# Kernel tuning notes

Measured on AMD Instinct MI355X. Metric: run time of the kernel, lower is better.

Reference implementation:

```python
import jax, jax.numpy as jnp
import numpy as np

D = 256        # d_model
NH = 8         # nhead
L = 2          # num_layers
FF = 1024      # dim_feedforward
HD = D // NH   # head dim
LN_EPS = 1e-5
M_EPS = 1e-9


def setup_inputs() -> dict:
    key = jax.random.key(0)
    ks = jax.random.split(key, 8)
    B, N, E = 8, 1024, 16384
    s = 0.02
    inp = {
        "H": jax.random.normal(ks[0], (B, N, D), jnp.float32),
        "edge_index": jax.random.randint(ks[1], (B, 2, E), 0, N),
        "m": jax.random.uniform(ks[2], (B, E), jnp.float32),
        # transformer encoder params, stacked over layers
        "Wqkv": jax.random.normal(ks[3], (L, 3 * D, D), jnp.float32) * s,
        "bqkv": jnp.zeros((L, 3 * D), jnp.float32),
        "Wo": jax.random.normal(ks[4], (L, D, D), jnp.float32) * s,
        "bo": jnp.zeros((L, D), jnp.float32),
        "ln1_w": jnp.ones((L, D), jnp.float32),
        "ln1_b": jnp.zeros((L, D), jnp.float32),
        "W1": jax.random.normal(ks[5], (L, FF, D), jnp.float32) * s,
        "b1": jnp.zeros((L, FF), jnp.float32),
        "W2": jax.random.normal(ks[6], (L, D, FF), jnp.float32) * s,
        "b2": jnp.zeros((L, D), jnp.float32),
        "ln2_w": jnp.ones((L, D), jnp.float32),
        "ln2_b": jnp.zeros((L, D), jnp.float32),
        "lnf_w": jnp.ones((D,), jnp.float32),
        "lnf_b": jnp.zeros((D,), jnp.float32),
    }
    return inp


def layer_norm(x, w, b):
    mu = jnp.mean(x, axis=-1, keepdims=True)
    var = jnp.mean(jnp.square(x - mu), axis=-1, keepdims=True)
    return (x - mu) * jax.lax.rsqrt(var + LN_EPS) * w + b


def build_bias(edge_index, m, N):
    # per-graph: -inf everywhere, 0 on diag, log(m+eps) symmetrically on edges
    bias = jnp.full((N, N), -jnp.inf, jnp.float32)
    d = jnp.arange(N)
    bias = bias.at[d, d].set(0.0)
    bv = jnp.log(m + M_EPS)
    row, col = edge_index[0], edge_index[1]
    bias = bias.at[row, col].set(bv)
    bias = bias.at[col, row].set(bv)
    return bias


def mha(x, bias, Wqkv, bqkv, Wo, bo):
    B, N, d = x.shape
    qkv = x @ Wqkv.T + bqkv                          # [B,N,3D]
    q, k, v = jnp.split(qkv, 3, axis=-1)
    def heads(t):
        return t.reshape(B, N, NH, HD).transpose(0, 2, 1, 3)  # [B,NH,N,HD]
    q, k, v = heads(q), heads(k), heads(v)
    scores = jnp.einsum("bhnd,bhmd->bhnm", q, k) / np.sqrt(HD)
    scores = scores + bias[:, None]                  # same bias for all heads
    attn = jax.nn.softmax(scores, axis=-1)
    out = jnp.einsum("bhnm,bhmd->bhnd", attn, v)
    out = out.transpose(0, 2, 1, 3).reshape(B, N, d)
    return out @ Wo.T + bo


def reference(H, edge_index, m, Wqkv, bqkv, Wo, bo, ln1_w, ln1_b, W1, b1,
              W2, b2, ln2_w, ln2_b, lnf_w, lnf_b):
    B, N, _ = H.shape
    bias = jax.vmap(lambda ei, mm: build_bias(ei, mm, N))(edge_index, m)  # [B,N,N]
    x = H
    for l in range(L):  # small fixed layer count
        a = mha(x, bias, Wqkv[l], bqkv[l], Wo[l], bo[l])
        x = layer_norm(x + a, ln1_w[l], ln1_b[l])
        f = jax.nn.gelu(x @ W1[l].T + b1[l], approximate=False) @ W2[l].T + b2[l]
        x = layer_norm(x + f, ln2_w[l], ln2_b[l])
    return layer_norm(x, lnf_w, lnf_b)
```

## Files before the change

kernel.cpp:

```cpp
#include <hip/hip_runtime.h>
#include <hip/hip_bf16.h>
#include <math.h>

typedef __bf16 bf16_t;
typedef __attribute__((ext_vector_type(8))) __bf16 bf16x8;
typedef __attribute__((ext_vector_type(4))) __bf16 bf16x4;
typedef __attribute__((ext_vector_type(4))) float f32x4;

#define BATCH 8
#define NTOK 1024
#define NEDGE 16384
#define CAP 96

__device__ __forceinline__ void gload_lds16(const void* g, void* l) {
  __builtin_amdgcn_global_load_lds(
      (const __attribute__((address_space(1))) unsigned int*)(uintptr_t)g,
      (__attribute__((address_space(3))) unsigned int*)(unsigned int)(uintptr_t)l,
      16, 0, 0);
}

__global__ void k_pre(int4* __restrict__ cnt,
                      const float* __restrict__ H, const float* __restrict__ Wqkv,
                      const float* __restrict__ Wo, const float* __restrict__ W1,
                      const float* __restrict__ W2, bf16_t* __restrict__ xb,
                      bf16_t* __restrict__ wqkvb, bf16_t* __restrict__ wob,
                      bf16_t* __restrict__ w1b, bf16_t* __restrict__ w2b) {
  int i = blockIdx.x * 256 + threadIdx.x;
  if (blockIdx.x < 8) {
    int4 z = {0, 0, 0, 0};
    cnt[i] = z;
  }
  const float* s; bf16_t* d; int off;
  if (i < 524288)      { s = H;    d = xb;    off = i; }
  else if (i < 622592) { s = Wqkv; d = wqkvb; off = i - 524288; }
  else if (i < 655360) { s = Wo;   d = wob;   off = i - 622592; }
  else if (i < 786432) { s = W1;   d = w1b;   off = i - 655360; }
  else if (i < 917504) { s = W2;   d = w2b;   off = i - 786432; }
  else return;
  float4 v = ((const float4*)s)[off];
  bf16x4 o;
  o[0] = (bf16_t)v.x; o[1] = (bf16_t)v.y; o[2] = (bf16_t)v.z; o[3] = (bf16_t)v.w;
  ((bf16x4*)d)[off] = o;
}

__global__ void k_scatter2(const int* __restrict__ ei, int* __restrict__ cnt,
                           int* __restrict__ ent) {
  int idx = blockIdx.x * 256 + threadIdx.x;
  if (idx >= BATCH * NEDGE) return;
  int b = idx >> 14;
  int e = idx & (NEDGE - 1);
  const int* eb = ei + (size_t)b * 2 * NEDGE;
  int r = eb[e], c = eb[NEDGE + e];
  int rowr = (b << 10) + r, rowc = (b << 10) + c;
  int q = atomicAdd(cnt + rowr, 1);
  if (q < CAP) ent[rowr * CAP + q] = ((e + 1) << 10) | c;
  q = atomicAdd(cnt + rowc, 1);
  if (q < CAP) ent[rowc * CAP + q] = ((NEDGE + e + 1) << 10) | r;
}

__global__ __launch_bounds__(256) void k_build2(
    const int* __restrict__ cnt, const int* __restrict__ ent,
    const float* __restrict__ mptr,
    int* __restrict__ nbcol, float* __restrict__ nbval, int* __restrict__ nbcnt) {
  const int w = threadIdx.x >> 6;
  const int l = threadIdx.x & 63;
  const int row = blockIdx.x * 4 + w;
  const int i = row & 1023;
  const int b = row >> 10;
  __shared__ int sE[4][CAP];
  __shared__ int sW[4][CAP];
  const int n = min(cnt[row], CAP);
  for (int j = l; j < n; j += 64) sE[w][j] = ent[(size_t)row * CAP + j];
  __syncthreads();

  bool dcov_l = false;
  bool win[2] = {false, false};
  int myc[2], myp[2];
#pragma unroll
  for (int s = 0; s < 2; ++s) {
    int k = s * 64 + l;
    if (k < n) {
      int pk = sE[w][k], ck = pk & 1023;
      myc[s] = ck; myp[s] = pk;
      bool wn = true;
      for (int j = 0; j < n; ++j) {
        int pj = sE[w][j];
        if ((pj & 1023) == ck && pj > pk) wn = false;
      }
      win[s] = wn;
      sW[w][k] = wn ? 1 : 0;
      if (ck == i) dcov_l = true;
    }
  }
  const bool dcov = __any(dcov_l);
  unsigned long long m0 = __ballot(win[0]);
  unsigned long long m1 = __ballot(win[1]);
  if (l == 0) nbcnt[row] = __popcll(m0) + __popcll(m1) + (dcov ? 0 : 1);

#pragma unroll
  for (int s = 0; s < 2; ++s) {
    int k = s * 64 + l;
    if (k < n && win[s]) {
      int pos = 0;
      for (int j = 0; j < n; ++j)
        if (sW[w][j] && (sE[w][j] & 1023) < myc[s]) ++pos;
      if (!dcov && i < myc[s]) ++pos;
      int e = ((myp[s] >> 10) - 1) & (NEDGE - 1);
      float v = logf(mptr[(size_t)b * NEDGE + e] + 1e-9f);
      if (pos < CAP) {
        nbcol[(size_t)row * CAP + pos] = myc[s];
        nbval[(size_t)row * CAP + pos] = v;
      }
    }
  }
  if (!dcov && l == 0) {
    int pos = 0;
    for (int j = 0; j < n; ++j)
      if (sW[w][j] && (sE[w][j] & 1023) < i) ++pos;
    nbcol[(size_t)row * CAP + pos] = i;
    nbval[(size_t)row * CAP + pos] = 0.f;
  }
}

template <int EPI, int BM>
__global__ __launch_bounds__(256) void gemm_bt(
    const bf16_t* __restrict__ A, const bf16_t* __restrict__ Bw,
    const float* __restrict__ bias, bf16_t* __restrict__ Cb,
    int M, int N, int K) {
  constexpr int MI = BM / 32;
  __shared__ bf16_t As[2][BM * 64];
  __shared__ bf16_t Bs[2][128 * 64];
  const int t = threadIdx.x;
  const int l = t & 63;
  const int w = t >> 6;
  const int wr = w >> 1, wc = w & 1;
  const int bm = blockIdx.y * BM, bn = blockIdx.x * 128;

  f32x4 acc[MI][4] = {};

  auto stage = [&](int buf, int k0) {
#pragma unroll
    for (int i = 0; i < BM / 32; ++i) {
      int idx = i * 2048 + t * 8;
      int row = idx >> 6, col = idx & 63;
      gload_lds16(A + (size_t)(bm + row) * K + (k0 + col), (void*)(&As[buf][0] + i * 2048 + w * 512));
    }
#pragma unroll
    for (int i = 0; i < 4; ++i) {
      int idx = i * 2048 + t * 8;
      int row = idx >> 6, col = idx & 63;
      gload_lds16(Bw + (size_t)(bn + row) * K + (k0 + col), (void*)(&Bs[buf][0] + i * 2048 + w * 512));
    }
  };

  const int nt = K >> 6;
  stage(0, 0);
  asm volatile("s_waitcnt vmcnt(0)" ::: "memory");
  __syncthreads();
  for (int kt = 0; kt < nt; ++kt) {
    const int cur = kt & 1;
    if (kt + 1 < nt) stage(cur ^ 1, (kt + 1) << 6);
#pragma unroll
    for (int kk = 0; kk < 2; ++kk) {
      bf16x8 af[MI], bfr[4];
#pragma unroll
      for (int mi = 0; mi < MI; ++mi)
        af[mi] = *(const bf16x8*)(&As[cur][0] + (wr * (BM / 2) + mi * 16 + (l & 15)) * 64 + kk * 32 + (l >> 4) * 8);
#pragma unroll
      for (int ni = 0; ni < 4; ++ni)
        bfr[ni] = *(const bf16x8*)(&Bs[cur][0] + (wc * 64 + ni * 16 + (l & 15)) * 64 + kk * 32 + (l >> 4) * 8);
#pragma unroll
      for (int mi = 0; mi < MI; ++mi)
#pragma unroll
        for (int ni = 0; ni < 4; ++ni)
          acc[mi][ni] = __builtin_amdgcn_mfma_f32_16x16x32_bf16(af[mi], bfr[ni], acc[mi][ni], 0, 0, 0);
    }
    asm volatile("s_waitcnt vmcnt(0)" ::: "memory");
    __syncthreads();
  }

  const int r0 = (l >> 4) * 4;
  const int cc = l & 15;
#pragma unroll
  for (int mi = 0; mi < MI; ++mi) {
#pragma unroll
    for (int ni = 0; ni < 4; ++ni) {
      int col = bn + wc * 64 + ni * 16 + cc;
      float bv = bias[col];
#pragma unroll
      for (int r = 0; r < 4; ++r) {
        int row = bm + wr * (BM / 2) + mi * 16 + r0 + r;
        float v = acc[mi][ni][r] + bv;
        if (EPI == 1)
          v = 0.5f * v * (1.f + erff(v * 0.70710678118654752f));
        Cb[(size_t)row * N + col] = (bf16_t)v;
      }
    }
  }
}

template <int FIN>
__global__ __launch_bounds__(256) void gemm_ln(
    const bf16_t* __restrict__ A, const bf16_t* __restrict__ Bw,
    const float* __restrict__ bias, const bf16_t* __restrict__ residb,
    const float* __restrict__ lnw, const float* __restrict__ lnb,
    const float* __restrict__ lnfw, const float* __restrict__ lnfb,
    bf16_t* __restrict__ xbout, float* __restrict__ outf, int K) {
  __shared__ __align__(16) char smem[69632];
  bf16_t* As = (bf16_t*)smem;
  bf16_t* Bs = (bf16_t*)(smem + 4096);
  float*  E  = (float*)smem;
  const int t = threadIdx.x;
  const int l = t & 63;
  const int w = t >> 6;
  const int bm = blockIdx.x * 16;

  f32x4 acc[4] = {};

  auto stage = [&](int buf, int k0) {
    if (w < 2) {
      int row = w * 8 + (l >> 3), col = (l & 7) * 8;
      gload_lds16(A + (size_t)(bm + row) * K + (k0 + col), (void*)(As + buf * 1024 + w * 512));
    }
#pragma unroll
    for (int i = 0; i < 8; ++i) {
      int rr = (w * 8 + i) * 8 + (l >> 3), col = (l & 7) * 8;
      gload_lds16(Bw + (size_t)rr * K + (k0 + col), (void*)(Bs + buf * 16384 + (w * 8 + i) * 512));
    }
  };

  const int nt = K >> 6;
  stage(0, 0);
  asm volatile("s_waitcnt vmcnt(0)" ::: "memory");
  __syncthreads();
  for (int kt = 0; kt < nt; ++kt) {
    const int cur = kt & 1;
    if (kt + 1 < nt) stage(cur ^ 1, (kt + 1) << 6);
#pragma unroll
    for (int kk = 0; kk < 2; ++kk) {
      bf16x8 af = *(const bf16x8*)(As + cur * 1024 + (l & 15) * 64 + kk * 32 + (l >> 4) * 8);
#pragma unroll
      for (int ni = 0; ni < 4; ++ni) {
        bf16x8 bfr = *(const bf16x8*)(Bs + cur * 16384 + (w * 64 + ni * 16 + (l & 15)) * 64 + kk * 32 + (l >> 4) * 8);
        acc[ni] = __builtin_amdgcn_mfma_f32_16x16x32_bf16(af, bfr, acc[ni], 0, 0, 0);
      }
    }
    asm volatile("s_waitcnt vmcnt(0)" ::: "memory");
    __syncthreads();
  }

  const int r0 = (l >> 4) * 4;
  const int cc = l & 15;
#pragma unroll
  for (int ni = 0; ni < 4; ++ni) {
    int col = w * 64 + ni * 16 + cc;
    float bv = bias[col];
#pragma unroll
    for (int r = 0; r < 4; ++r)
      E[(r0 + r) * 258 + col] = acc[ni][r] + bv;
  }
  __syncthreads();

  const int row = t >> 4;
  const int sub = t & 15;
  const float* ep = E + row * 258 + sub * 16;
  const bf16_t* rp = residb + (size_t)(bm + row) * 256 + sub * 16;
  float v[16];
  float s = 0.f;
#pragma unroll
  for (int j = 0; j < 4; ++j) {
    float4 a4 = ((const float4*)ep)[j];
    bf16x4 r4 = ((const bf16x4*)rp)[j];
    v[j * 4 + 0] = a4.x + (float)r4[0]; v[j * 4 + 1] = a4.y + (float)r4[1];
    v[j * 4 + 2] = a4.z + (float)r4[2]; v[j * 4 + 3] = a4.w + (float)r4[3];
    s += v[j * 4 + 0] + v[j * 4 + 1] + v[j * 4 + 2] + v[j * 4 + 3];
  }
#pragma unroll
  for (int o = 1; o < 16; o <<= 1) s += __shfl_xor(s, o);
  float mu = s * (1.f / 256.f);
  float e2 = 0.f;
#pragma unroll
  for (int j = 0; j < 16; ++j) { float d = v[j] - mu; e2 += d * d; }
#pragma unroll
  for (int o = 1; o < 16; o <<= 1) e2 += __shfl_xor(e2, o);
  float rs = rsqrtf(e2 * (1.f / 256.f) + 1e-5f);
  float y[16];
#pragma unroll
  for (int j = 0; j < 4; ++j) {
    float4 w4 = ((const float4*)(lnw + sub * 16))[j];
    float4 b4 = ((const float4*)(lnb + sub * 16))[j];
    y[j * 4 + 0] = (v[j * 4 + 0] - mu) * rs * w4.x + b4.x;
    y[j * 4 + 1] = (v[j * 4 + 1] - mu) * rs * w4.y + b4.y;
    y[j * 4 + 2] = (v[j * 4 + 2] - mu) * rs * w4.z + b4.z;
    y[j * 4 + 3] = (v[j * 4 + 3] - mu) * rs * w4.w + b4.w;
  }
  if (FIN == 0) {
    bf16_t* xbo = xbout + (size_t)(bm + row) * 256 + sub * 16;
#pragma unroll
    for (int j = 0; j < 4; ++j) {
      bf16x4 ob;
      ob[0] = (bf16_t)y[j * 4 + 0]; ob[1] = (bf16_t)y[j * 4 + 1];
      ob[2] = (bf16_t)y[j * 4 + 2]; ob[3] = (bf16_t)y[j * 4 + 3];
      ((bf16x4*)xbo)[j] = ob;
    }
  } else {
    float s2 = 0.f;
#pragma unroll
    for (int j = 0; j < 16; ++j) s2 += y[j];
#pragma unroll
    for (int o = 1; o < 16; o <<= 1) s2 += __shfl_xor(s2, o);
    float mu2 = s2 * (1.f / 256.f);
    float q2 = 0.f;
#pragma unroll
    for (int j = 0; j < 16; ++j) { float d = y[j] - mu2; q2 += d * d; }
#pragma unroll
    for (int o = 1; o < 16; o <<= 1) q2 += __shfl_xor(q2, o);
    float rs2 = rsqrtf(q2 * (1.f / 256.f) + 1e-5f);
    float* xo = outf + (size_t)(bm + row) * 256 + sub * 16;
#pragma unroll
    for (int j = 0; j < 4; ++j) {
      float4 w4 = ((const float4*)(lnfw + sub * 16))[j];
      float4 b4 = ((const float4*)(lnfb + sub * 16))[j];
      float4 o4 = {(y[j * 4 + 0] - mu2) * rs2 * w4.x + b4.x,
                   (y[j * 4 + 1] - mu2) * rs2 * w4.y + b4.y,
                   (y[j * 4 + 2] - mu2) * rs2 * w4.z + b4.z,
                   (y[j * 4 + 3] - mu2) * rs2 * w4.w + b4.w};
      ((float4*)xo)[j] = o4;
    }
  }
}

__global__ __launch_bounds__(256) void k_attn2(
    const bf16_t* __restrict__ qkvb,
    const int* __restrict__ nbcol, const float* __restrict__ nbval,
    const int* __restrict__ nbcnt, bf16_t* __restrict__ aob) {
  const int w = threadIdx.x >> 6;
  const int l = threadIdx.x & 63;
  const int b = blockIdx.x & 7;
  const int row = (b << 10) + (blockIdx.x >> 3) * 4 + w;
  __shared__ float s_s[4][8][97];
  __shared__ int   s_col[4][CAP];
  __shared__ float s_bias[4][CAP];
  __shared__ float s_den[4][8];
  const int deg = nbcnt[row];
  for (int j = l; j < deg; j += 64) {
    s_col[w][j] = nbcol[(size_t)row * CAP + j];
    s_bias[w][j] = nbval[(size_t)row * CAP + j];
  }
  const int h1 = l & 7;
  float q[32];
  {
    const bf16x8* qp = (const bf16x8*)(qkvb + (size_t)row * 768 + h1 * 32);
#pragma unroll
    for (int u = 0; u < 4; ++u) {
      bf16x8 t8 = qp[u];
#pragma unroll
      for (int j = 0; j < 8; ++j) q[u * 8 + j] = (float)t8[j];
    }
  }
  __syncthreads();

  const float scale = 0.17677669529663687f;
  const int nit = (deg + 7) >> 3;
  float mx = -INFINITY;
  for (int it = 0; it < nit; ++it) {
    int idx = it * 8 + (l >> 3);
    float sc = -INFINITY;
    if (idx < deg) {
      int col = s_col[w][idx];
      const bf16x8* kr = (const bf16x8*)(qkvb + ((size_t)((b << 10) + col)) * 768 + 256 + h1 * 32);
      float d = 0.f;
#pragma unroll
      for (int u = 0; u < 4; ++u) {
        bf16x8 kv = kr[u];
#pragma unroll
        for (int j = 0; j < 8; ++j) d += (float)kv[j] * q[u * 8 + j];
      }
      sc = d * scale + s_bias[w][idx];
      s_s[w][h1][idx] = sc;
    }
    mx = fmaxf(mx, sc);
  }
#pragma unroll
  for (int o = 8; o < 64; o <<= 1) mx = fmaxf(mx, __shfl_xor(mx, o));
  __syncthreads();
  float lsum = 0.f;
  for (int it = 0; it < nit; ++it) {
    int idx = it * 8 + (l >> 3);
    if (idx < deg) {
      float p = __expf(s_s[w][h1][idx] - mx);
      s_s[w][h1][idx] = p;
      lsum += p;
    }
  }
#pragma unroll
  for (int o = 8; o < 64; o <<= 1) lsum += __shfl_xor(lsum, o);
  if (l < 8) s_den[w][l] = lsum;
  __syncthreads();
  const int h3 = l >> 3;
  float a0 = 0.f, a1 = 0.f, a2 = 0.f, a3 = 0.f;
  const bf16_t* vbase = qkvb + ((size_t)(b << 10)) * 768 + 512 + l * 4;
#pragma unroll 4
  for (int idx = 0; idx < deg; ++idx) {
    float p = s_s[w][h3][idx];
    bf16x4 vv = *(const bf16x4*)(vbase + (size_t)s_col[w][idx] * 768);
    a0 += p * (float)vv[0]; a1 += p * (float)vv[1];
    a2 += p * (float)vv[2]; a3 += p * (float)vv[3];
  }
  float rden = 1.f / s_den[w][h3];
  bf16x4 o;
  o[0] = (bf16_t)(a0 * rden); o[1] = (bf16_t)(a1 * rden);
  o[2] = (bf16_t)(a2 * rden); o[3] = (bf16_t)(a3 * rden);
  *(bf16x4*)(aob + (size_t)row * 256 + l * 4) = o;
}

extern "C" void kernel_launch(void* const* d_in, const int* in_sizes, int n_in,
                              void* d_out, int out_size, void* d_ws, size_t ws_size,
                              hipStream_t stream) {
  const float* H    = (const float*)d_in[0];
  const int*   ei   = (const int*)d_in[1];
  const float* m    = (const float*)d_in[2];
  const float* Wqkv = (const float*)d_in[3];
  const float* bqkv = (const float*)d_in[4];
  const float* Wo   = (const float*)d_in[5];
  const float* bo   = (const float*)d_in[6];
  const float* ln1w = (const float*)d_in[7];
  const float* ln1b = (const float*)d_in[8];
  const float* W1   = (const float*)d_in[9];
  const float* b1   = (const float*)d_in[10];
  const float* W2   = (const float*)d_in[11];
  const float* b2   = (const float*)d_in[12];
  const float* ln2w = (const float*)d_in[13];
  const float* ln2b = (const float*)d_in[14];
  const float* lnfw = (const float*)d_in[15];
  const float* lnfb = (const float*)d_in[16];

  char* ws = (char*)d_ws;
  size_t off = 0;
  auto alloc = [&](size_t bytes) {
    void* p = ws + off;
    off += (bytes + 255) & ~(size_t)255;
    return p;
  };

  int*    cnt   = (int*)alloc((size_t)BATCH * NTOK * 4);
  int*    ent   = (int*)alloc((size_t)BATCH * NTOK * CAP * 4);
  int*    nbcol = (int*)alloc((size_t)BATCH * NTOK * CAP * 4);
  float*  nbval = (float*)alloc((size_t)BATCH * NTOK * CAP * 4);
  int*    nbcnt = (int*)alloc((size_t)BATCH * NTOK * 4);
  bf16_t* qkvb  = (bf16_t*)alloc((size_t)8192 * 768 * 2);
  bf16_t* wqkvb = (bf16_t*)alloc((size_t)2 * 768 * 256 * 2);
  bf16_t* wob   = (bf16_t*)alloc((size_t)2 * 256 * 256 * 2);
  bf16_t* w1b   = (bf16_t*)alloc((size_t)2 * 1024 * 256 * 2);
  bf16_t* w2b   = (bf16_t*)alloc((size_t)2 * 256 * 1024 * 2);
  bf16_t* xb    = (bf16_t*)alloc((size_t)8192 * 256 * 2);
  bf16_t* x1b   = (bf16_t*)alloc((size_t)8192 * 256 * 2);
  bf16_t* aob   = (bf16_t*)alloc((size_t)8192 * 256 * 2);
  bf16_t* ffb   = (bf16_t*)alloc((size_t)8192 * 1024 * 2);

  k_pre<<<3584, 256, 0, stream>>>((int4*)cnt, H, Wqkv, Wo, W1, W2,
                                  xb, wqkvb, wob, w1b, w2b);
  k_scatter2<<<(BATCH * NEDGE + 255) / 256, 256, 0, stream>>>(ei, cnt, ent);
  k_build2<<<BATCH * NTOK / 4, 256, 0, stream>>>(cnt, ent, m, nbcol, nbval, nbcnt);

  for (int lyr = 0; lyr < 2; ++lyr) {
    gemm_bt<3, 64><<<dim3(768 / 128, 8192 / 64), 256, 0, stream>>>(
        xb, wqkvb + (size_t)lyr * 768 * 256, bqkv + lyr * 768, qkvb, 8192, 768, 256);
    k_attn2<<<BATCH * NTOK / 4, 256, 0, stream>>>(qkvb, nbcol, nbval, nbcnt, aob);
    gemm_ln<0><<<512, 256, 0, stream>>>(
        aob, wob + (size_t)lyr * 256 * 256, bo + lyr * 256, xb,
        ln1w + lyr * 256, ln1b + lyr * 256, nullptr, nullptr, x1b, nullptr, 256);
    gemm_bt<1, 128><<<dim3(1024 / 128, 8192 / 128), 256, 0, stream>>>(
        x1b, w1b + (size_t)lyr * 1024 * 256, b1 + lyr * 1024, ffb, 8192, 1024, 256);
    if (lyr == 0) {
      gemm_ln<0><<<512, 256, 0, stream>>>(
          ffb, w2b + (size_t)lyr * 256 * 1024, b2 + lyr * 256, x1b,
          ln2w + lyr * 256, ln2b + lyr * 256, nullptr, nullptr, xb, nullptr, 1024);
    } else {
      gemm_ln<1><<<512, 256, 0, stream>>>(
          ffb, w2b + (size_t)lyr * 256 * 1024, b2 + lyr * 256, x1b,
          ln2w + lyr * 256, ln2b + lyr * 256, lnfw, lnfb, nullptr, (float*)d_out, 1024);
    }
  }
}
```

Baseline: 197.9 us.

## Fuse sparse attention with output projection, residual and LayerNorm

```diff
diff --git a/kernel.cpp b/kernel.cpp
--- a/kernel.cpp
+++ b/kernel.cpp
@@ -196,6 +196,179 @@
         Cb[(size_t)row * N + col] = (bf16_t)v;
       }
     }
+  }
+}
+
+__global__ __launch_bounds__(256) void k_attn_oproj(
+    const bf16_t* __restrict__ qkvb,
+    const int* __restrict__ nbcol, const float* __restrict__ nbval,
+    const int* __restrict__ nbcnt,
+    const bf16_t* __restrict__ Wo, const float* __restrict__ bo,
+    const bf16_t* __restrict__ residb,
+    const float* __restrict__ lnw, const float* __restrict__ lnb,
+    bf16_t* __restrict__ xbout) {
+  __shared__ __align__(16) char smem[57856];
+  bf16_t* Bs    = (bf16_t*)smem;
+  bf16_t* ao    = (bf16_t*)(smem + 32768);
+  float*  s_s   = (float*)(smem + 41216);
+  int*    s_col = (int*)(smem + 53632);
+  float*  s_bia = (float*)(smem + 55168);
+  float*  E     = (float*)(smem + 41216);
+  const int t = threadIdx.x, l = t & 63, w = t >> 6;
+  const int b = blockIdx.x & 7;
+  const int bm = (b << 10) + (blockIdx.x >> 3) * 16;
+
+  auto stageB = [&](int k0) {
+#pragma unroll
+    for (int i = 0; i < 8; ++i) {
+      int rr = (w * 8 + i) * 8 + (l >> 3), col = (l & 7) * 8;
+      gload_lds16(Wo + (size_t)rr * 256 + (k0 + col), (void*)(Bs + (w * 8 + i) * 512));
+    }
+  };
+  stageB(0);
+
+  const float scale = 0.17677669529663687f;
+  const int h1 = l & 7;
+  for (int rr = 0; rr < 4; ++rr) {
+    const int row = bm + w * 4 + rr;
+    const int deg = nbcnt[row];
+    asm volatile("s_waitcnt lgkmcnt(0)" ::: "memory");
+    for (int j = l; j < deg; j += 64) {
+      s_col[w * 96 + j] = nbcol[(size_t)row * CAP + j];
+      s_bia[w * 96 + j] = nbval[(size_t)row * CAP + j];
+    }
+    float q[32];
+    {
+      const bf16x8* qp = (const bf16x8*)(qkvb + (size_t)row * 768 + h1 * 32);
+#pragma unroll
+      for (int u = 0; u < 4; ++u) {
+        bf16x8 t8 = qp[u];
+#pragma unroll
+        for (int j = 0; j < 8; ++j) q[u * 8 + j] = (float)t8[j];
+      }
+    }
+    asm volatile("s_waitcnt lgkmcnt(0)" ::: "memory");
+
+    const int nit = (deg + 7) >> 3;
+    float mx = -INFINITY;
+    for (int it = 0; it < nit; ++it) {
+      int idx = it * 8 + (l >> 3);
+      float sc = -INFINITY;
+      if (idx < deg) {
+        int col = s_col[w * 96 + idx];
+        const bf16x8* kr = (const bf16x8*)(qkvb + ((size_t)((b << 10) + col)) * 768 + 256 + h1 * 32);
+        float d = 0.f;
+#pragma unroll
+        for (int u = 0; u < 4; ++u) {
+          bf16x8 kv = kr[u];
+#pragma unroll
+          for (int j = 0; j < 8; ++j) d += (float)kv[j] * q[u * 8 + j];
+        }
+        sc = d * scale + s_bia[w * 96 + idx];
+        s_s[(w * 8 + h1) * 97 + idx] = sc;
+      }
+      mx = fmaxf(mx, sc);
+    }
+#pragma unroll
+    for (int o = 8; o < 64; o <<= 1) mx = fmaxf(mx, __shfl_xor(mx, o));
+    asm volatile("s_waitcnt lgkmcnt(0)" ::: "memory");
+    float lsum = 0.f;
+    for (int it = 0; it < nit; ++it) {
+      int idx = it * 8 + (l >> 3);
+      if (idx < deg) {
+        float p = __expf(s_s[(w * 8 + h1) * 97 + idx] - mx);
+        s_s[(w * 8 + h1) * 97 + idx] = p;
+        lsum += p;
+      }
+    }
+#pragma unroll
+    for (int o = 8; o < 64; o <<= 1) lsum += __shfl_xor(lsum, o);
+    const int h3 = l >> 3;
+    float den = __shfl(lsum, h3);
+    asm volatile("s_waitcnt lgkmcnt(0)" ::: "memory");
+    float a0 = 0.f, a1 = 0.f, a2 = 0.f, a3 = 0.f;
+    const bf16_t* vbase = qkvb + ((size_t)(b << 10)) * 768 + 512 + l * 4;
+#pragma unroll 4
+    for (int idx = 0; idx < deg; ++idx) {
+      float p = s_s[(w * 8 + h3) * 97 + idx];
+      bf16x4 vv = *(const bf16x4*)(vbase + (size_t)s_col[w * 96 + idx] * 768);
+      a0 += p * (float)vv[0]; a1 += p * (float)vv[1];
+      a2 += p * (float)vv[2]; a3 += p * (float)vv[3];
+    }
+    float rden = 1.f / den;
+    bf16x4 o4;
+    o4[0] = (bf16_t)(a0 * rden); o4[1] = (bf16_t)(a1 * rden);
+    o4[2] = (bf16_t)(a2 * rden); o4[3] = (bf16_t)(a3 * rden);
+    *(bf16x4*)(ao + (w * 4 + rr) * 264 + l * 4) = o4;
+  }
+  asm volatile("s_waitcnt vmcnt(0) lgkmcnt(0)" ::: "memory");
+  __syncthreads();
+
+  f32x4 acc[4] = {};
+  for (int kt = 0; kt < 4; ++kt) {
+#pragma unroll
+    for (int kk = 0; kk < 2; ++kk) {
+      bf16x8 af = *(const bf16x8*)(ao + (l & 15) * 264 + kt * 64 + kk * 32 + (l >> 4) * 8);
+#pragma unroll
+      for (int ni = 0; ni < 4; ++ni) {
+        bf16x8 bfr = *(const bf16x8*)(Bs + (w * 64 + ni * 16 + (l & 15)) * 64 + kk * 32 + (l >> 4) * 8);
+        acc[ni] = __builtin_amdgcn_mfma_f32_16x16x32_bf16(af, bfr, acc[ni], 0, 0, 0);
+      }
+    }
+    __syncthreads();
+    if (kt < 3) {
+      stageB((kt + 1) * 64);
+      asm volatile("s_waitcnt vmcnt(0)" ::: "memory");
+      __syncthreads();
+    }
+  }
+
+  const int r0 = (l >> 4) * 4;
+  const int cc = l & 15;
+#pragma unroll
+  for (int ni = 0; ni < 4; ++ni) {
+    int col = w * 64 + ni * 16 + cc;
+    float bv = bo[col];
+#pragma unroll
+    for (int r = 0; r < 4; ++r)
+      E[(r0 + r) * 258 + col] = acc[ni][r] + bv;
+  }
+  __syncthreads();
+
+  const int row = t >> 4;
+  const int sub = t & 15;
+  const float* ep = E + row * 258 + sub * 16;
+  const bf16_t* rp = residb + (size_t)(bm + row) * 256 + sub * 16;
+  float v[16];
+  float s = 0.f;
+#pragma unroll
+  for (int j = 0; j < 4; ++j) {
+    float4 a4 = ((const float4*)ep)[j];
+    bf16x4 r4 = ((const bf16x4*)rp)[j];
+    v[j * 4 + 0] = a4.x + (float)r4[0]; v[j * 4 + 1] = a4.y + (float)r4[1];
+    v[j * 4 + 2] = a4.z + (float)r4[2]; v[j * 4 + 3] = a4.w + (float)r4[3];
+    s += v[j * 4 + 0] + v[j * 4 + 1] + v[j * 4 + 2] + v[j * 4 + 3];
+  }
+#pragma unroll
+  for (int o = 1; o < 16; o <<= 1) s += __shfl_xor(s, o);
+  float mu = s * (1.f / 256.f);
+  float e2 = 0.f;
+#pragma unroll
+  for (int j = 0; j < 16; ++j) { float d = v[j] - mu; e2 += d * d; }
+#pragma unroll
+  for (int o = 1; o < 16; o <<= 1) e2 += __shfl_xor(e2, o);
+  float rs = rsqrtf(e2 * (1.f / 256.f) + 1e-5f);
+  bf16_t* xbo = xbout + (size_t)(bm + row) * 256 + sub * 16;
+#pragma unroll
+  for (int j = 0; j < 4; ++j) {
+    float4 w4 = ((const float4*)(lnw + sub * 16))[j];
+    float4 b4 = ((const float4*)(lnb + sub * 16))[j];
+    bf16x4 ob;
+    ob[0] = (bf16_t)((v[j * 4 + 0] - mu) * rs * w4.x + b4.x);
+    ob[1] = (bf16_t)((v[j * 4 + 1] - mu) * rs * w4.y + b4.y);
+    ob[2] = (bf16_t)((v[j * 4 + 2] - mu) * rs * w4.z + b4.z);
+    ob[3] = (bf16_t)((v[j * 4 + 3] - mu) * rs * w4.w + b4.w);
+    ((bf16x4*)xbo)[j] = ob;
   }
 }
 
@@ -328,90 +501,6 @@
       ((float4*)xo)[j] = o4;
     }
   }
-}
-
-__global__ __launch_bounds__(256) void k_attn2(
-    const bf16_t* __restrict__ qkvb,
-    const int* __restrict__ nbcol, const float* __restrict__ nbval,
-    const int* __restrict__ nbcnt, bf16_t* __restrict__ aob) {
-  const int w = threadIdx.x >> 6;
-  const int l = threadIdx.x & 63;
-  const int b = blockIdx.x & 7;
-  const int row = (b << 10) + (blockIdx.x >> 3) * 4 + w;
-  __shared__ float s_s[4][8][97];
-  __shared__ int   s_col[4][CAP];
-  __shared__ float s_bias[4][CAP];
-  __shared__ float s_den[4][8];
-  const int deg = nbcnt[row];
-  for (int j = l; j < deg; j += 64) {
-    s_col[w][j] = nbcol[(size_t)row * CAP + j];
-    s_bias[w][j] = nbval[(size_t)row * CAP + j];
-  }
-  const int h1 = l & 7;
-  float q[32];
-  {
-    const bf16x8* qp = (const bf16x8*)(qkvb + (size_t)row * 768 + h1 * 32);
-#pragma unroll
-    for (int u = 0; u < 4; ++u) {
-      bf16x8 t8 = qp[u];
-#pragma unroll
-      for (int j = 0; j < 8; ++j) q[u * 8 + j] = (float)t8[j];
-    }
-  }
-  __syncthreads();
-
-  const float scale = 0.17677669529663687f;
-  const int nit = (deg + 7) >> 3;
-  float mx = -INFINITY;
-  for (int it = 0; it < nit; ++it) {
-    int idx = it * 8 + (l >> 3);
-    float sc = -INFINITY;
-    if (idx < deg) {
-      int col = s_col[w][idx];
-      const bf16x8* kr = (const bf16x8*)(qkvb + ((size_t)((b << 10) + col)) * 768 + 256 + h1 * 32);
-      float d = 0.f;
-#pragma unroll
-      for (int u = 0; u < 4; ++u) {
-        bf16x8 kv = kr[u];
-#pragma unroll
-        for (int j = 0; j < 8; ++j) d += (float)kv[j] * q[u * 8 + j];
-      }
-      sc = d * scale + s_bias[w][idx];
-      s_s[w][h1][idx] = sc;
-    }
-    mx = fmaxf(mx, sc);
-  }
-#pragma unroll
-  for (int o = 8; o < 64; o <<= 1) mx = fmaxf(mx, __shfl_xor(mx, o));
-  __syncthreads();
-  float lsum = 0.f;
-  for (int it = 0; it < nit; ++it) {
-    int idx = it * 8 + (l >> 3);
-    if (idx < deg) {
-      float p = __expf(s_s[w][h1][idx] - mx);
-      s_s[w][h1][idx] = p;
-      lsum += p;
-    }
-  }
-#pragma unroll
-  for (int o = 8; o < 64; o <<= 1) lsum += __shfl_xor(lsum, o);
-  if (l < 8) s_den[w][l] = lsum;
-  __syncthreads();
-  const int h3 = l >> 3;
-  float a0 = 0.f, a1 = 0.f, a2 = 0.f, a3 = 0.f;
-  const bf16_t* vbase = qkvb + ((size_t)(b << 10)) * 768 + 512 + l * 4;
-#pragma unroll 4
-  for (int idx = 0; idx < deg; ++idx) {
-    float p = s_s[w][h3][idx];
-    bf16x4 vv = *(const bf16x4*)(vbase + (size_t)s_col[w][idx] * 768);
-    a0 += p * (float)vv[0]; a1 += p * (float)vv[1];
-    a2 += p * (float)vv[2]; a3 += p * (float)vv[3];
-  }
-  float rden = 1.f / s_den[w][h3];
-  bf16x4 o;
-  o[0] = (bf16_t)(a0 * rden); o[1] = (bf16_t)(a1 * rden);
-  o[2] = (bf16_t)(a2 * rden); o[3] = (bf16_t)(a3 * rden);
-  *(bf16x4*)(aob + (size_t)row * 256 + l * 4) = o;
 }
 
 extern "C" void kernel_launch(void* const* d_in, const int* in_sizes, int n_in,
@@ -455,7 +544,6 @@
   bf16_t* w2b   = (bf16_t*)alloc((size_t)2 * 256 * 1024 * 2);
   bf16_t* xb    = (bf16_t*)alloc((size_t)8192 * 256 * 2);
   bf16_t* x1b   = (bf16_t*)alloc((size_t)8192 * 256 * 2);
-  bf16_t* aob   = (bf16_t*)alloc((size_t)8192 * 256 * 2);
   bf16_t* ffb   = (bf16_t*)alloc((size_t)8192 * 1024 * 2);
 
   k_pre<<<3584, 256, 0, stream>>>((int4*)cnt, H, Wqkv, Wo, W1, W2,
@@ -466,10 +554,10 @@
   for (int lyr = 0; lyr < 2; ++lyr) {
     gemm_bt<3, 64><<<dim3(768 / 128, 8192 / 64), 256, 0, stream>>>(
         xb, wqkvb + (size_t)lyr * 768 * 256, bqkv + lyr * 768, qkvb, 8192, 768, 256);
-    k_attn2<<<BATCH * NTOK / 4, 256, 0, stream>>>(qkvb, nbcol, nbval, nbcnt, aob);
-    gemm_ln<0><<<512, 256, 0, stream>>>(
-        aob, wob + (size_t)lyr * 256 * 256, bo + lyr * 256, xb,
-        ln1w + lyr * 256, ln1b + lyr * 256, nullptr, nullptr, x1b, nullptr, 256);
+    k_attn_oproj<<<512, 256, 0, stream>>>(
+        qkvb, nbcol, nbval, nbcnt,
+        wob + (size_t)lyr * 256 * 256, bo + lyr * 256, xb,
+        ln1w + lyr * 256, ln1b + lyr * 256, x1b);
     gemm_bt<1, 128><<<dim3(1024 / 128, 8192 / 128), 256, 0, stream>>>(
         x1b, w1b + (size_t)lyr * 1024 * 256, b1 + lyr * 1024, ffb, 8192, 1024, 256);
     if (lyr == 0) {
```

After: 195.1 us, median of 2. Within noise of the previous version (-1.4%).
